# Optimization experiments

Hardware: AMD Instinct MI355X
Metric: run time of the kernel (lower is better)

Reference implementation:

```python
import jax, jax.numpy as jnp
import numpy as np

B, T, E = 64, 1024, 2048  # BATCH_SIZE, TRAIN_LEN, EMBEDDING_LEN (E > T branch, as in repo configs)


def setup_inputs() -> dict:
    key = jax.random.key(0)
    delay_embedding = jax.random.normal(key, (B, T, E), dtype=jnp.float32)
    return {"delay_embedding": delay_embedding}


def reference(delay_embedding):
    """Hankel anti-diagonal segmented mean (embedding_2_predict_y, all_y=False).

    delay_embedding: [B, T, E]. Elements with equal index-sum s = i + j lie on the
    same anti-diagonal; the torch code averages each such diagonal. With
    all_y=False it returns diagonals s = T .. T+E-2  ->  output shape [B, E-1].
    One fused segment_sum pass replaces the per-batch, per-diagonal python loops.
    """
    Bv, Tv, Ev = delay_embedding.shape
    S = Tv + Ev - 1  # number of anti-diagonals
    seg = (jnp.arange(Tv)[:, None] + jnp.arange(Ev)[None, :]).reshape(-1)  # [T*E]
    data = delay_embedding.reshape(Bv, Tv * Ev).T  # [T*E, B], segments on axis 0
    sums = jax.ops.segment_sum(data, seg, num_segments=S)  # [S, B]
    counts = jax.ops.segment_sum(jnp.ones((Tv * Ev,), jnp.float32), seg, num_segments=S)  # [S]
    means = (sums / counts[:, None]).T  # [B, S]
    return means[:, Tv:]  # [B, E-1]
```

## Files before the change

### kernel.cpp

```cpp
#include <hip/hip_runtime.h>


#define T_LEN 1024
#define E_LEN 2048
#define K_OUT (E_LEN - 1)
#define B_SZ  64
#define NSPLIT 4
#define CHUNK (T_LEN / NSPLIT)

__global__ void __launch_bounds__(256)
diag_accum(const float* __restrict__ in, float* __restrict__ out) {
    const int k = blockIdx.x * blockDim.x + threadIdx.x;
    if (k >= K_OUT) return;
    const int b = blockIdx.y;
    const int z = blockIdx.z;

    int i_lo = z * CHUNK;
    const int i_hi = i_lo + CHUNK;
    const int k_lo = k - (T_LEN - 1);
    if (k_lo > i_lo) i_lo = k_lo;
    if (i_lo >= i_hi) return;

    const int over = k - (T_LEN - 1);
    const int cnt = T_LEN - (over > 0 ? over : 0);
    const float scale = 1.0f / (float)cnt;

    const float* p = in + (size_t)b * T_LEN * E_LEN
                        + (size_t)i_lo * (E_LEN - 1)
                        + (size_t)(T_LEN + k);
    float s = 0.0f;
    #pragma unroll 16
    for (int i = i_lo; i < i_hi; ++i) {
        s += *p;
        p += (E_LEN - 1);
    }
    atomicAdd(&out[(size_t)b * K_OUT + k], s * scale);
}

extern "C" void kernel_launch(void* const* d_in, const int* in_sizes, int n_in,
                              void* d_out, int out_size, void* d_ws, size_t ws_size,
                              hipStream_t stream) {
    const float* in = (const float*)d_in[0];
    float* out = (float*)d_out;

    hipMemsetAsync(out, 0, sizeof(float) * B_SZ * K_OUT, stream);

    dim3 grid((K_OUT + 255) / 256, B_SZ, NSPLIT);
    diag_accum<<<grid, 256, 0, stream>>>(in, out);
}
```

Measured before the change: 102.5 us.

## Process four adjacent diagonals per thread with vector loads and flattened grid

New measurement: 94.65 us. 7.6% less time.

```diff
diff --git a/kernel.cpp b/kernel.cpp
--- a/kernel.cpp
+++ b/kernel.cpp
@@ -5,36 +5,64 @@
 #define E_LEN 2048
 #define K_OUT (E_LEN - 1)
 #define B_SZ  64
-#define NSPLIT 4
-#define CHUNK (T_LEN / NSPLIT)
+#define NZ    4
+#define ROWS  (T_LEN / NZ)
+#define TPB   128
+#define NBLK  (NZ * B_SZ * 4)
 
-__global__ void __launch_bounds__(256)
+__global__ void __launch_bounds__(TPB)
 diag_accum(const float* __restrict__ in, float* __restrict__ out) {
-    const int k = blockIdx.x * blockDim.x + threadIdx.x;
-    if (k >= K_OUT) return;
-    const int b = blockIdx.y;
-    const int z = blockIdx.z;
+    const int bid  = blockIdx.x;
+    const int zraw = bid & (NZ - 1);
+    const int b    = (bid >> 2) & (B_SZ - 1);
+    const int x    = bid >> 8;
 
-    int i_lo = z * CHUNK;
-    const int i_hi = i_lo + CHUNK;
-    const int k_lo = k - (T_LEN - 1);
-    if (k_lo > i_lo) i_lo = k_lo;
-    if (i_lo >= i_hi) return;
+    int z = zraw;
+    if (x == 3) z = (zraw < 2) ? (3 - zraw) : (zraw - 2);
 
-    const int over = k - (T_LEN - 1);
-    const int cnt = T_LEN - (over > 0 ? over : 0);
-    const float scale = 1.0f / (float)cnt;
+    const int g  = x * TPB + threadIdx.x;
+    const int k0 = g << 2;
+    const int r0 = z * ROWS;
+    const int r1 = r0 + ROWS;
+
+    const int il0 = max(r0, k0     - (T_LEN - 1));
+    const int il3 = max(r0, k0 + 3 - (T_LEN - 1));
+    if (il0 >= r1) return;
 
     const float* p = in + (size_t)b * T_LEN * E_LEN
-                        + (size_t)i_lo * (E_LEN - 1)
-                        + (size_t)(T_LEN + k);
-    float s = 0.0f;
-    #pragma unroll 16
-    for (int i = i_lo; i < i_hi; ++i) {
-        s += *p;
+                        + (size_t)il0 * (E_LEN - 1)
+                        + (size_t)(T_LEN + k0);
+    float sx = 0.f, sy = 0.f, sz = 0.f, sw = 0.f;
+    int i = il0;
+
+    const int head_end = min(il3, r1);
+    for (; i < head_end; ++i) {
+        sx += p[0];
+        if (i >= k0 + 1 - (T_LEN - 1)) sy += p[1];
+        if (i >= k0 + 2 - (T_LEN - 1)) sz += p[2];
         p += (E_LEN - 1);
     }
-    atomicAdd(&out[(size_t)b * K_OUT + k], s * scale);
+
+    #pragma unroll 8
+    for (; i < r1; ++i) {
+        float v[4];
+        __builtin_memcpy(v, p, 16);
+        sx += v[0]; sy += v[1]; sz += v[2]; sw += v[3];
+        p += (E_LEN - 1);
+    }
+
+    const int ov = k0 - (T_LEN - 1);
+    const float n0 = (float)(T_LEN - max(0, ov));
+    const float n1 = (float)(T_LEN - max(0, ov + 1));
+    const float n2 = (float)(T_LEN - max(0, ov + 2));
+    float* o = out + (size_t)b * K_OUT + k0;
+    atomicAdd(o + 0, sx * (1.0f / n0));
+    atomicAdd(o + 1, sy * (1.0f / n1));
+    atomicAdd(o + 2, sz * (1.0f / n2));
+    if (k0 + 3 < K_OUT) {
+        const float n3 = (float)(T_LEN - max(0, ov + 3));
+        atomicAdd(o + 3, sw * (1.0f / n3));
+    }
 }
 
 extern "C" void kernel_launch(void* const* d_in, const int* in_sizes, int n_in,
@@ -45,6 +73,5 @@
 
     hipMemsetAsync(out, 0, sizeof(float) * B_SZ * K_OUT, stream);
 
-    dim3 grid((K_OUT + 255) / 256, B_SZ, NSPLIT);
-    diag_accum<<<grid, 256, 0, stream>>>(in, out);
+    diag_accum<<<NBLK, TPB, 0, stream>>>(in, out);
 }
```

## Stream rows coalesced into per-wave LDS diagonal accumulators

Applied to the files above, without the earlier changes.

New measurement: 97.28 us. 1.05x faster.

```diff
diff --git a/kernel.cpp b/kernel.cpp
--- a/kernel.cpp
+++ b/kernel.cpp
@@ -5,36 +5,57 @@
 #define E_LEN 2048
 #define K_OUT (E_LEN - 1)
 #define B_SZ  64
-#define NSPLIT 4
-#define CHUNK (T_LEN / NSPLIT)
+#define NP    16
+#define NBLK  (NP * B_SZ)
+#define LSTR  2080
 
 __global__ void __launch_bounds__(256)
 diag_accum(const float* __restrict__ in, float* __restrict__ out) {
-    const int k = blockIdx.x * blockDim.x + threadIdx.x;
-    if (k >= K_OUT) return;
-    const int b = blockIdx.y;
-    const int z = blockIdx.z;
+    __shared__ float lacc[4][LSTR];
 
-    int i_lo = z * CHUNK;
-    const int i_hi = i_lo + CHUNK;
-    const int k_lo = k - (T_LEN - 1);
-    if (k_lo > i_lo) i_lo = k_lo;
-    if (i_lo >= i_hi) return;
+    const int b    = blockIdx.x & (B_SZ - 1);
+    const int p    = blockIdx.x >> 6;
+    const int w    = threadIdx.x >> 6;
+    const int lane = threadIdx.x & 63;
 
-    const int over = k - (T_LEN - 1);
-    const int cnt = T_LEN - (over > 0 ? over : 0);
-    const float scale = 1.0f / (float)cnt;
+    float* acc = lacc[w];
+    for (int t = lane; t < LSTR; t += 64) acc[t] = 0.0f;
 
-    const float* p = in + (size_t)b * T_LEN * E_LEN
-                        + (size_t)i_lo * (E_LEN - 1)
-                        + (size_t)(T_LEN + k);
-    float s = 0.0f;
-    #pragma unroll 16
-    for (int i = i_lo; i < i_hi; ++i) {
-        s += *p;
-        p += (E_LEN - 1);
+    const float* inb = in + (size_t)b * T_LEN * E_LEN;
+
+    for (int r = 0; r < 16; ++r) {
+        const int i = (r < 8) ? (32 * p + 8 * w + r)
+                              : (992 - 32 * p + 8 * (3 - w) + (r - 8));
+        const int jmin = T_LEN - i;
+        const int jb   = jmin & ~31;
+        const int kofs = i - T_LEN + 32;
+        const float* rowp = inb + (size_t)i * E_LEN;
+
+        #pragma unroll 2
+        for (int j4 = jb + 4 * lane; j4 < E_LEN; j4 += 256) {
+            float v[4];
+            __builtin_memcpy(v, rowp + j4, 16);
+            float* a = &acc[j4 + kofs];
+            const float a0 = a[0], a1 = a[1], a2 = a[2], a3 = a[3];
+            a[0] = a0 + ((j4 + 0 >= jmin) ? v[0] : 0.0f);
+            a[1] = a1 + ((j4 + 1 >= jmin) ? v[1] : 0.0f);
+            a[2] = a2 + ((j4 + 2 >= jmin) ? v[2] : 0.0f);
+            a[3] = a3 + ((j4 + 3 >= jmin) ? v[3] : 0.0f);
+        }
     }
-    atomicAdd(&out[(size_t)b * K_OUT + k], s * scale);
+
+    __syncthreads();
+
+    #pragma unroll
+    for (int m = 0; m < 8; ++m) {
+        const int k = (int)threadIdx.x + 256 * (m ^ (p & 7));
+        if (k < K_OUT) {
+            const float v = lacc[0][k + 32] + lacc[1][k + 32]
+                          + lacc[2][k + 32] + lacc[3][k + 32];
+            const int cnt = T_LEN - max(0, k - (T_LEN - 1));
+            unsafeAtomicAdd(&out[(size_t)b * K_OUT + k], v * (1.0f / (float)cnt));
+        }
+    }
 }
 
 extern "C" void kernel_launch(void* const* d_in, const int* in_sizes, int n_in,
@@ -45,6 +66,5 @@
 
     hipMemsetAsync(out, 0, sizeof(float) * B_SZ * K_OUT, stream);
 
-    dim3 grid((K_OUT + 255) / 256, B_SZ, NSPLIT);
-    diag_accum<<<grid, 256, 0, stream>>>(in, out);
+    diag_accum<<<NBLK, 256, 0, stream>>>(in, out);
 }
```
